# Kernel optimization log

Measured on AMD Instinct MI355X. Metric: run time of the kernel, lower is better.

Reference implementation:

```python
import jax, jax.numpy as jnp
import numpy as np

DIM = 50
K = 51  # kernel_size == DIM + 1 (required by the original view())
E = 6   # num_elems
NT = 29 # num_targets
B = 8
DN = ('NCDHW', 'OIDHW', 'NCDHW')


def setup_inputs() -> dict:
    key = jax.random.key(0)
    ks = jax.random.split(key, 14)
    f = jnp.float32
    inp = {
        'x': jax.random.uniform(ks[0], (B, E, DIM, DIM, DIM), dtype=f),
        'sigma': 3.0 * jnp.ones((E,), dtype=f),
        'w1': jax.random.normal(ks[1], (32, E, 3, 3, 3), dtype=f) * 0.1,
        'b1': jnp.full((32,), 0.01, dtype=f),
        'w2': jax.random.normal(ks[2], (64, 32, 3, 3, 3), dtype=f) * 0.05,
        'b2': jnp.full((64,), 0.01, dtype=f),
        'w3': jax.random.normal(ks[3], (128, 64, 3, 3, 3), dtype=f) * 0.05,
        'b3': jnp.full((128,), 0.01, dtype=f),
        'w4': jax.random.normal(ks[4], (256, 128, 3, 3, 3), dtype=f) * 0.03,
        'b4': jnp.full((256,), 0.01, dtype=f),
        'fw1': jax.random.normal(ks[5], (128, 256), dtype=f) * 0.06,
        'fb1': jnp.full((128,), 0.01, dtype=f),
        'fw2': jax.random.normal(ks[6], (NT, 128), dtype=f) * 0.08,
        'fb2': jnp.full((NT,), 0.01, dtype=f),
    }
    return inp


def _blur_kernel(sigma):
    # Gauss transformation kernel, shape (E, 1, K, K, K)
    c = jnp.arange(K, dtype=jnp.float32)
    mean = (K - 1) / 2.0
    d2 = (c - mean) ** 2
    # squared radius grid (K,K,K), symmetric so the torch transpose(3,0) axis swap is a no-op
    r2 = d2[:, None, None] + d2[None, :, None] + d2[None, None, :]
    var = sigma ** 2  # (E,)
    a = 1.0 / (2.0 * np.pi * var)  # (E,)
    kern = a[:, None, None, None] * jnp.exp(-r2[None] / (2.0 * var)[:, None, None, None])
    kern = kern / jnp.sum(kern)  # normalize by GLOBAL sum (as in torch code)
    return kern[:, None]  # (E,1,K,K,K)


def _conv3(x, w, b):
    y = jax.lax.conv_general_dilated(x, w, (1, 1, 1), 'VALID', dimension_numbers=DN)
    return y + b[None, :, None, None, None]


def _pool(x):
    return jax.lax.reduce_window(x, -jnp.inf, jax.lax.max,
                                 (1, 1, 2, 2, 2), (1, 1, 2, 2, 2), 'VALID')


def reference(x, sigma, w1, b1, w2, b2, w3, b3, w4, b4, fw1, fb1, fw2, fb2):
    # blur: grouped 3D conv with on-the-fly Gaussian kernel, padding 25 keeps DIM
    kern = _blur_kernel(sigma)
    pad = (K - 1) // 2
    xc = jax.lax.conv_general_dilated(x, kern, (1, 1, 1), [(pad, pad)] * 3,
                                      feature_group_count=E, dimension_numbers=DN)
    xc = xc / jnp.max(xc)
    # conv stack: (conv -> pool -> relu) x4
    h = jax.nn.relu(_pool(_conv3(xc, w1, b1)))   # (B,32,24,24,24)
    h = jax.nn.relu(_pool(_conv3(h, w2, b2)))    # (B,64,11,11,11)
    h = jax.nn.relu(_pool(_conv3(h, w3, b3)))    # (B,128,4,4,4)
    h = jax.nn.relu(_pool(_conv3(h, w4, b4)))    # (B,256,1,1,1)
    v = h.reshape(x.shape[0], -1)                # (B,256)
    y1 = jax.nn.relu(v @ fw1.T + fb1)
    return y1 @ fw2.T + fb2                      # (B,29)
```

## Files before the change

kernel.cpp:

```cpp
#include <hip/hip_runtime.h>
#include <math.h>

#define DIMX 50
#define KK   51
#define NE   6
#define NB   8
#define NVOX ((size_t)NB * NE * DIMX * DIMX * DIMX)

typedef short bf16x8 __attribute__((ext_vector_type(8)));
typedef float f32x4  __attribute__((ext_vector_type(4)));

__device__ __forceinline__ unsigned short f2bf(float f) {
    unsigned u = __float_as_uint(f);
    u += 0x7fffu + ((u >> 16) & 1u);
    return (unsigned short)(u >> 16);
}
__device__ __forceinline__ float bf2f(unsigned short h) {
    return __uint_as_float((unsigned)h << 16);
}
__device__ __forceinline__ uint4 pack8(const unsigned short v[8]) {
    uint4 q;
    q.x = v[0] | ((unsigned)v[1] << 16);
    q.y = v[2] | ((unsigned)v[3] << 16);
    q.z = v[4] | ((unsigned)v[5] << 16);
    q.w = v[6] | ((unsigned)v[7] << 16);
    return q;
}
__device__ __forceinline__ void split2(float v0, float v1, unsigned& hp, unsigned& lp) {
    unsigned u0 = __float_as_uint(v0), u1 = __float_as_uint(v1);
    float h0 = __uint_as_float(u0 & 0xffff0000u);
    float h1 = __uint_as_float(u1 & 0xffff0000u);
    hp = __builtin_amdgcn_perm(u1, u0, 0x07060302u);
    lp = __builtin_amdgcn_perm(__float_as_uint(v1 - h1), __float_as_uint(v0 - h0), 0x07060302u);
}
__device__ __forceinline__ int offA(int o, int k) {
    return ((((o >> 4) * 2 + (k >> 5)) * 64 + ((k >> 3) & 3) * 16 + (o & 15)) << 3) + (k & 7);
}

__global__ void taps_kernel(const float* __restrict__ sigma,
                            unsigned short* __restrict__ MA, unsigned short* __restrict__ MB,
                            float* __restrict__ maxval) {
    __shared__ float sg[NE * KK];
    __shared__ float sgs[NE * KK];
    __shared__ float ssum[NE];
    int t = threadIdx.x;
    if (t == 0) *maxval = 0.f;
    if (t < NE * KK) {
        int e = t / KK, i = t % KK;
        float d = (float)i - 25.0f;
        float var = sigma[e] * sigma[e];
        sg[t] = expf(-d * d / (2.f * var));
    }
    __syncthreads();
    if (t < NE) {
        float s = 0.f;
        for (int i = 0; i < KK; ++i) s += sg[t * KK + i];
        ssum[t] = s;
    }
    __syncthreads();
    if (t < NE * KK) {
        int e = t / KK;
        float S = 0.f;
        for (int e2 = 0; e2 < NE; ++e2) {
            float var2 = sigma[e2] * sigma[e2];
            float a2 = 1.f / (2.f * (float)M_PI * var2);
            float se = ssum[e2];
            S += a2 * se * se * se;
        }
        float var = sigma[e] * sigma[e];
        float a = 1.f / (2.f * (float)M_PI * var);
        sgs[t] = sg[t] * (a / S);
    }
    __syncthreads();
    const int TOT = 2 * 6 * 4 * 2 * 64 * 8;
    for (int i = t; i < 2 * TOT; i += 512) {
        int which = i / TOT;
        int r = i % TOT;
        int q = r;
        int j = q & 7; q >>= 3;
        int l = q & 63; q >>= 6;
        int kc = q & 1; q >>= 1;
        int tile = q & 3; q >>= 2;
        int e = q % 6; q /= 6;
        int hl = q;
        int own = tile * 16 + (l & 15);
        int k   = kc * 32 + ((l >> 4) << 3) + j;
        float v = 0.f;
        if (own < 50 && k < 50) {
            int d = k - own + 25;
            if (d >= 0 && d < KK) v = (which == 0 ? sg : sgs)[e * KK + d];
        }
        unsigned short h = f2bf(v);
        unsigned short out = (hl == 0) ? h : f2bf(v - bf2f(h));
        (which == 0 ? MA : MB)[r] = out;
    }
}

__global__ __launch_bounds__(64)
void blur_k1(const float* __restrict__ in, float* __restrict__ W1,
             const unsigned short* __restrict__ MA) {
    const int l = threadIdx.x, lm = l & 15, lg = l >> 4;
    const int y = blockIdx.x % 50, be = blockIdx.x / 50, e = be % 6;
    const float* pb = in + (size_t)be * 125000 + y * 50;
    bf16x8 Ah[4][2], Al[4][2];
#pragma unroll
    for (int ozt = 0; ozt < 4; ++ozt)
#pragma unroll
        for (int kc = 0; kc < 2; ++kc) {
            Ah[ozt][kc] = *(const bf16x8*)(MA + (((size_t)(0 * 6 + e) * 4 + ozt) * 2 + kc) * 512 + l * 8);
            Al[ozt][kc] = *(const bf16x8*)(MA + (((size_t)(1 * 6 + e) * 4 + ozt) * 2 + kc) * 512 + l * 8);
        }
    float* ob = W1 + (size_t)be * 125000 + y * 50;
    const f32x4 z4 = {0.f, 0.f, 0.f, 0.f};
#pragma unroll
    for (int xt = 0; xt < 4; ++xt) {
        const int xx = xt * 16 + lm;
        bf16x8 bh[2], bl[2];
#pragma unroll
        for (int kc = 0; kc < 2; ++kc) {
            float v[8];
#pragma unroll
            for (int j = 0; j < 8; ++j) {
                int z = kc * 32 + lg * 8 + j;
                v[j] = (z < 50 && xx < 50) ? pb[(size_t)z * 2500 + xx] : 0.f;
            }
            uint4 qh, ql;
            split2(v[0], v[1], qh.x, ql.x);
            split2(v[2], v[3], qh.y, ql.y);
            split2(v[4], v[5], qh.z, ql.z);
            split2(v[6], v[7], qh.w, ql.w);
            bh[kc] = *(bf16x8*)&qh; bl[kc] = *(bf16x8*)&ql;
        }
        f32x4 acc[4];
#pragma unroll
        for (int ozt = 0; ozt < 4; ++ozt) acc[ozt] = z4;
#pragma unroll
        for (int ozt = 0; ozt < 4; ++ozt)
#pragma unroll
            for (int kc = 0; kc < 2; ++kc) {
                acc[ozt] = __builtin_amdgcn_mfma_f32_16x16x32_bf16(Ah[ozt][kc], bh[kc], acc[ozt], 0, 0, 0);
                acc[ozt] = __builtin_amdgcn_mfma_f32_16x16x32_bf16(Ah[ozt][kc], bl[kc], acc[ozt], 0, 0, 0);
                acc[ozt] = __builtin_amdgcn_mfma_f32_16x16x32_bf16(Al[ozt][kc], bh[kc], acc[ozt], 0, 0, 0);
            }
        if (xx < 50) {
#pragma unroll
            for (int ozt = 0; ozt < 4; ++ozt)
#pragma unroll
                for (int i = 0; i < 4; ++i) {
                    int oz = ozt * 16 + lg * 4 + i;
                    if (oz < 50) ob[(size_t)oz * 2500 + xx] = acc[ozt][i];
                }
        }
    }
}

__global__ __launch_bounds__(64)
void blur_k2(const float* __restrict__ W1, const unsigned short* __restrict__ MA,
             const unsigned short* __restrict__ MB, unsigned short* __restrict__ X1,
             float* __restrict__ maxval) {
    __shared__ unsigned short Qhi[4096], Qlo[4096];
    const int l = threadIdx.x, lm = l & 15, lg = (l >> 4);
    const int q8 = (int)(gridDim.x >> 3);
    const int logical = ((int)blockIdx.x & 7) * q8 + ((int)blockIdx.x >> 3);
    const int e = logical % 6, bz = logical / 6, z = bz % 50, b = bz / 50;
    const float* pb = W1 + (size_t)(b * 6 + e) * 125000 + (size_t)z * 2500;
    bf16x8 Bh[4][2], Bl[4][2];
#pragma unroll
    for (int xt = 0; xt < 4; ++xt) {
        const int xx = xt * 16 + lm;
#pragma unroll
        for (int kc = 0; kc < 2; ++kc) {
            float v[8];
#pragma unroll
            for (int j = 0; j < 8; ++j) {
                int yy = kc * 32 + lg * 8 + j;
                v[j] = (yy < 50 && xx < 50) ? pb[yy * 50 + xx] : 0.f;
            }
            uint4 qh, ql;
            split2(v[0], v[1], qh.x, ql.x);
            split2(v[2], v[3], qh.y, ql.y);
            split2(v[4], v[5], qh.z, ql.z);
            split2(v[6], v[7], qh.w, ql.w);
            Bh[xt][kc] = *(bf16x8*)&qh; Bl[xt][kc] = *(bf16x8*)&ql;
        }
    }
    const f32x4 z4 = {0.f, 0.f, 0.f, 0.f};
#pragma unroll
    for (int oyt = 0; oyt < 4; ++oyt) {
        bf16x8 Ah[2], Al[2];
#pragma unroll
        for (int kc = 0; kc < 2; ++kc) {
            Ah[kc] = *(const bf16x8*)(MA + (((size_t)(0 * 6 + e) * 4 + oyt) * 2 + kc) * 512 + l * 8);
            Al[kc] = *(const bf16x8*)(MA + (((size_t)(1 * 6 + e) * 4 + oyt) * 2 + kc) * 512 + l * 8);
        }
#pragma unroll
        for (int xt = 0; xt < 4; ++xt) {
            f32x4 acc = z4;
#pragma unroll
            for (int kc = 0; kc < 2; ++kc) {
                acc = __builtin_amdgcn_mfma_f32_16x16x32_bf16(Ah[kc], Bh[xt][kc], acc, 0, 0, 0);
                acc = __builtin_amdgcn_mfma_f32_16x16x32_bf16(Ah[kc], Bl[xt][kc], acc, 0, 0, 0);
                acc = __builtin_amdgcn_mfma_f32_16x16x32_bf16(Al[kc], Bh[xt][kc], acc, 0, 0, 0);
            }
#pragma unroll
            for (int i = 0; i < 4; ++i) {
                int oy = oyt * 16 + lg * 4 + i;
                int xx = xt * 16 + lm;
                float qv = acc[i];
                unsigned u = __float_as_uint(qv);
                int off = offA(oy, xx);
                Qhi[off] = (unsigned short)(u >> 16);
                float lo = qv - __uint_as_float(u & 0xffff0000u);
                Qlo[off] = (unsigned short)(__float_as_uint(lo) >> 16);
            }
        }
    }
    __builtin_amdgcn_wave_barrier();
    asm volatile("s_waitcnt lgkmcnt(0)" ::: "memory");
    __builtin_amdgcn_sched_barrier(0);
    float mmax = 0.f;
    unsigned short* xb = X1 + ((size_t)b * 125000 + (size_t)z * 2500) * 8 + e;
#pragma unroll
    for (int oyt = 0; oyt < 4; ++oyt) {
        bf16x8 Qh[2], Ql[2];
#pragma unroll
        for (int kc = 0; kc < 2; ++kc) {
            Qh[kc] = *(const bf16x8*)(Qhi + ((oyt * 2 + kc) * 64 + l) * 8);
            Ql[kc] = *(const bf16x8*)(Qlo + ((oyt * 2 + kc) * 64 + l) * 8);
        }
#pragma unroll
        for (int oxt = 0; oxt < 4; ++oxt) {
            f32x4 acc = z4;
#pragma unroll
            for (int kc = 0; kc < 2; ++kc) {
                bf16x8 mh = *(const bf16x8*)(MB + (((size_t)(0 * 6 + e) * 4 + oxt) * 2 + kc) * 512 + l * 8);
                bf16x8 ml = *(const bf16x8*)(MB + (((size_t)(1 * 6 + e) * 4 + oxt) * 2 + kc) * 512 + l * 8);
                acc = __builtin_amdgcn_mfma_f32_16x16x32_bf16(Qh[kc], mh, acc, 0, 0, 0);
                acc = __builtin_amdgcn_mfma_f32_16x16x32_bf16(Qh[kc], ml, acc, 0, 0, 0);
                acc = __builtin_amdgcn_mfma_f32_16x16x32_bf16(Ql[kc], mh, acc, 0, 0, 0);
            }
            int ox = oxt * 16 + lm;
            if (ox < 50) {
#pragma unroll
                for (int i = 0; i < 4; ++i) {
                    int oy = oyt * 16 + lg * 4 + i;
                    if (oy < 50) {
                        float r = acc[i];
                        xb[((size_t)oy * 50 + ox) * 8] = f2bf(r);
                        mmax = fmaxf(mmax, r);
                    }
                }
            }
        }
    }
    for (int o = 32; o; o >>= 1) mmax = fmaxf(mmax, __shfl_xor(mmax, o));
    if (l == 0) atomicMax((int*)maxval, __float_as_int(mmax));
}

__global__ void wprep_all(const float* __restrict__ W1c, const float* __restrict__ W2c,
                          const float* __restrict__ W3c,
                          unsigned short* __restrict__ wp1, unsigned short* __restrict__ wp2,
                          unsigned short* __restrict__ wp3) {
    int idx = blockIdx.x * 256 + threadIdx.x;
    const int N1 = 2 * 9 * 64;
    const int N2 = 4 * 27 * 1 * 64;
    const int N3 = 8 * 27 * 2 * 64;
    if (idx < N1) {
        int l = idx & 63;
        int r = idx >> 6;
        int tg = r % 9, cog = r / 9;
        int xsel = l >> 4;
        int co = cog * 16 + (l & 15);
        unsigned short v[8];
#pragma unroll
        for (int j = 0; j < 8; ++j) {
            float wv = 0.f;
            if (j < 6 && xsel < 3) wv = W1c[((size_t)co * 6 + j) * 27 + tg * 3 + xsel];
            v[j] = f2bf(wv);
        }
        ((uint4*)wp1)[idx] = pack8(v);
        return;
    }
    idx -= N1;
    if (idx < N2) {
        int l = idx & 63;
        int r = idx >> 6;
        int tap = r % 27, cog = r / 27;
        int co = cog * 16 + (l & 15);
        unsigned short v[8];
#pragma unroll
        for (int j = 0; j < 8; ++j) {
            int ci = (l >> 4) * 8 + j;
            v[j] = f2bf(W2c[((size_t)co * 32 + ci) * 27 + tap]);
        }
        ((uint4*)wp2)[idx] = pack8(v);
        return;
    }
    idx -= N2;
    if (idx < N3) {
        int l = idx & 63;
        int r = idx >> 6;
        int ch = r % 2; r /= 2;
        int tap = r % 27;
        int cog = r / 27;
        int co = cog * 16 + (l & 15);
        unsigned short v[8];
#pragma unroll
        for (int j = 0; j < 8; ++j) {
            int ci = ch * 32 + (l >> 4) * 8 + j;
            v[j] = f2bf(W3c[((size_t)co * 64 + ci) * 27 + tap]);
        }
        ((uint4*)wp3)[idx] = pack8(v);
    }
}

__global__ __launch_bounds__(64, 3)
void conv1_mfma(const unsigned short* __restrict__ X8, const unsigned short* __restrict__ wp1,
                const float* __restrict__ bias, const float* __restrict__ maxval,
                unsigned short* __restrict__ X2) {
    const int l = threadIdx.x, lm = l & 15, lg = l >> 4;
    const int q = (int)(gridDim.x >> 3);
    const int bid = ((int)blockIdx.x & 7) * q + ((int)blockIdx.x >> 3);
    const int s0 = bid * 8;
    const int r0 = s0 / 72;
    const int cog = r0 % 2;
    const int pz  = (r0 / 2) % 24;
    const int b   = r0 / 48;
    uint4 B9[9];
    const uint4* wpb = (const uint4*)wp1 + cog * 9 * 64;
#pragma unroll
    for (int t = 0; t < 9; ++t) B9[t] = wpb[t * 64 + l];
    const float rmv = 1.0f / (*maxval);
    const float bia = bias[cog * 16 + lm];
    const unsigned short* Xb = X8 + (size_t)b * 125000 * 8;
    const f32x4 z4 = {0.f, 0.f, 0.f, 0.f};
#pragma unroll 1
    for (int si = 0; si < 8; ++si) {
        const int sid = s0 + si;
        const int xs = sid % 3;
        const int py = (sid / 3) % 24;
        const int x0 = xs * 16;
        f32x4 acc[2][2];
#pragma unroll
        for (int cz = 0; cz < 2; ++cz)
#pragma unroll
            for (int cy = 0; cy < 2; ++cy) acc[cz][cy] = z4;
#pragma unroll
        for (int zi = 0; zi < 4; ++zi) {
            const int zin = 2 * pz + zi;
#pragma unroll
            for (int yi = 0; yi < 4; ++yi) {
                const int yin = 2 * py + yi;
                const unsigned short* rowb = Xb + (size_t)(zin * 50 + yin) * 50 * 8;
                bf16x8 a = *(const bf16x8*)(rowb + (x0 + lm + lg) * 8);
#pragma unroll
                for (int cz = 0; cz < 2; ++cz) {
                    const int kz = zi - cz;
                    if (kz < 0 || kz > 2) continue;
#pragma unroll
                    for (int cy = 0; cy < 2; ++cy) {
                        const int ky = yi - cy;
                        if (ky < 0 || ky > 2) continue;
                        acc[cz][cy] = __builtin_amdgcn_mfma_f32_16x16x32_bf16(
                            a, *(const bf16x8*)&B9[kz * 3 + ky], acc[cz][cy], 0, 0, 0);
                    }
                }
            }
        }
        const int co = cog * 16 + lm;
#pragma unroll
        for (int ip = 0; ip < 2; ++ip) {
            float m0 = fmaxf(fmaxf(acc[0][0][2 * ip], acc[0][1][2 * ip]),
                             fmaxf(acc[1][0][2 * ip], acc[1][1][2 * ip]));
            float m1 = fmaxf(fmaxf(acc[0][0][2 * ip + 1], acc[0][1][2 * ip + 1]),
                             fmaxf(acc[1][0][2 * ip + 1], acc[1][1][2 * ip + 1]));
            float o = fmaxf(fmaxf(m0, m1) * rmv + bia, 0.f);
            int px = x0 / 2 + lg * 2 + ip;
            X2[((((size_t)b * 24 + pz) * 24 + py) * 24 + px) * 32 + co] = f2bf(o);
        }
    }
}

template <int DIN, int DP, int CI, int NCH, int NCOG, int NPY, int NXS, int SPB, int NPZ>
__global__ __launch_bounds__(64, 3)
void convN_mfma(const unsigned short* __restrict__ X, const unsigned short* __restrict__ wp,
                const float* __restrict__ bias, unsigned short* __restrict__ Y, int COUT) {
    const int l = threadIdx.x, lm = l & 15, lg = l >> 4;
    const int qq = (int)(gridDim.x >> 3);
    const int bid = ((int)blockIdx.x & 7) * qq + ((int)blockIdx.x >> 3);
    const int s0 = bid * SPB;
    const int r0 = s0 / (NPY * NXS);
    const int cog = r0 % NCOG;
    const int pz  = (r0 / NCOG) % NPZ;
    const int b   = r0 / (NCOG * NPZ);
    const float bia = bias[cog * 16 + lm];
    const unsigned short* Xb = X + (size_t)b * DIN * DIN * DIN * CI;
    const uint4* wp4 = (const uint4*)wp;
    const f32x4 z4 = {0.f, 0.f, 0.f, 0.f};
#pragma unroll 1
    for (int si = 0; si < SPB; ++si) {
        const int sid = s0 + si;
        const int xs = sid % NXS;
        const int py = (sid / NXS) % NPY;
        const int x0 = xs * 16;
        int xo[3];
#pragma unroll
        for (int kx = 0; kx < 3; ++kx) {
            int xin = x0 + kx + lm;
            if (xin > DIN - 1) xin = DIN - 1;
            xo[kx] = xin * CI + lg * 8;
        }
        f32x4 acc[2][2];
#pragma unroll
        for (int cz = 0; cz < 2; ++cz)
#pragma unroll
            for (int cy = 0; cy < 2; ++cy) acc[cz][cy] = z4;
#pragma unroll 1
        for (int ch = 0; ch < NCH; ++ch) {
            uint4 B[27];
            const uint4* wpb = wp4 + ((size_t)cog * 27 * NCH + ch) * 64;
#pragma unroll
            for (int t = 0; t < 27; ++t) B[t] = wpb[(size_t)t * NCH * 64 + l];
            const unsigned short* Xc = Xb + ch * 32;
#pragma unroll
            for (int zi = 0; zi < 4; ++zi) {
                const int zin = 2 * pz + zi;
#pragma unroll
                for (int yi = 0; yi < 4; ++yi) {
                    const int yin = 2 * py + yi;
                    const unsigned short* rowb = Xc + (size_t)(zin * DIN + yin) * DIN * CI;
#pragma unroll
                    for (int kx = 0; kx < 3; ++kx) {
                        bf16x8 a = *(const bf16x8*)(rowb + xo[kx]);
#pragma unroll
                        for (int cz = 0; cz < 2; ++cz) {
                            const int kz = zi - cz;
                            if (kz < 0 || kz > 2) continue;
#pragma unroll
                            for (int cy = 0; cy < 2; ++cy) {
                                const int ky = yi - cy;
                                if (ky < 0 || ky > 2) continue;
                                const int tap = (kz * 3 + ky) * 3 + kx;
                                acc[cz][cy] = __builtin_amdgcn_mfma_f32_16x16x32_bf16(
                                    a, *(const bf16x8*)&B[tap], acc[cz][cy], 0, 0, 0);
                            }
                        }
                    }
                }
            }
        }
        const int co = cog * 16 + lm;
#pragma unroll
        for (int ip = 0; ip < 2; ++ip) {
            float m0 = fmaxf(fmaxf(acc[0][0][2 * ip], acc[0][1][2 * ip]),
                             fmaxf(acc[1][0][2 * ip], acc[1][1][2 * ip]));
            float m1 = fmaxf(fmaxf(acc[0][0][2 * ip + 1], acc[0][1][2 * ip + 1]),
                             fmaxf(acc[1][0][2 * ip + 1], acc[1][1][2 * ip + 1]));
            float o = fmaxf(fmaxf(m0, m1) + bia, 0.f);
            int px = x0 / 2 + lg * 2 + ip;
            if (px < DP)
                Y[((((size_t)b * DP + pz) * DP + py) * DP + px) * COUT + co] = f2bf(o);
        }
    }
}

__global__ void conv4_kernel(const unsigned short* __restrict__ X4, const float* __restrict__ w,
                             const float* __restrict__ bias, float* __restrict__ out) {
    int wid = (int)((blockIdx.x * blockDim.x + threadIdx.x) >> 6);
    int lane = threadIdx.x & 63;
    if (wid >= NB * 256) return;
    int b = wid >> 8, co = wid & 255;
    float acc[8];
#pragma unroll
    for (int i = 0; i < 8; ++i) acc[i] = 0.f;
    for (int half = 0; half < 2; ++half) {
        int ci = lane + half * 64;
        float win[64];
#pragma unroll
        for (int v = 0; v < 64; ++v)
            win[v] = bf2f(X4[((size_t)b * 64 + v) * 128 + ci]);
        const float* wc = w + ((size_t)co * 128 + ci) * 27;
        float wr[27];
#pragma unroll
        for (int i = 0; i < 27; ++i) wr[i] = wc[i];
#pragma unroll
        for (int kz = 0; kz < 3; ++kz)
#pragma unroll
            for (int ky = 0; ky < 3; ++ky)
#pragma unroll
                for (int kx = 0; kx < 3; ++kx) {
                    float wv = wr[(kz * 3 + ky) * 3 + kx];
#pragma unroll
                    for (int oz = 0; oz < 2; ++oz)
#pragma unroll
                        for (int oy = 0; oy < 2; ++oy)
#pragma unroll
                            for (int ox = 0; ox < 2; ++ox)
                                acc[(oz * 2 + oy) * 2 + ox] =
                                    fmaf(wv, win[((oz + kz) * 4 + (oy + ky)) * 4 + ox + kx],
                                         acc[(oz * 2 + oy) * 2 + ox]);
                }
    }
#pragma unroll
    for (int o = 32; o; o >>= 1)
#pragma unroll
        for (int i = 0; i < 8; ++i) acc[i] += __shfl_xor(acc[i], o);
    if (lane == 0) {
        float m = acc[0];
#pragma unroll
        for (int i = 1; i < 8; ++i) m = fmaxf(m, acc[i]);
        out[(size_t)b * 256 + co] = fmaxf(m + bias[co], 0.f);
    }
}

__global__ void head_kernel(const float* __restrict__ v,
                            const float* __restrict__ fw1, const float* __restrict__ fb1,
                            const float* __restrict__ fw2, const float* __restrict__ fb2,
                            float* __restrict__ out) {
    int b = blockIdx.x, t = threadIdx.x;
    __shared__ float sv[256];
    __shared__ float s1[128];
    sv[t] = v[b * 256 + t];
    sv[t + 128] = v[b * 256 + t + 128];
    __syncthreads();
    float acc = fb1[t];
    const float* wr = fw1 + t * 256;
    for (int k = 0; k < 256; ++k) acc = fmaf(wr[k], sv[k], acc);
    s1[t] = fmaxf(acc, 0.f);
    __syncthreads();
    if (t < 29) {
        float a2 = fb2[t];
        const float* w2 = fw2 + t * 128;
        for (int k = 0; k < 128; ++k) a2 = fmaf(w2[k], s1[k], a2);
        out[b * 29 + t] = a2;
    }
}

extern "C" void kernel_launch(void* const* d_in, const int* in_sizes, int n_in,
                              void* d_out, int out_size, void* d_ws, size_t ws_size,
                              hipStream_t stream) {
    const float* x     = (const float*)d_in[0];
    const float* sigma = (const float*)d_in[1];
    const float* w1    = (const float*)d_in[2];
    const float* b1    = (const float*)d_in[3];
    const float* w2    = (const float*)d_in[4];
    const float* b2    = (const float*)d_in[5];
    const float* w3    = (const float*)d_in[6];
    const float* b3    = (const float*)d_in[7];
    const float* w4    = (const float*)d_in[8];
    const float* b4    = (const float*)d_in[9];
    const float* fw1   = (const float*)d_in[10];
    const float* fb1   = (const float*)d_in[11];
    const float* fw2   = (const float*)d_in[12];
    const float* fb2   = (const float*)d_in[13];
    float* out = (float*)d_out;

    float* W1 = (float*)d_ws;
    unsigned short* X1  = (unsigned short*)(W1 + NVOX);
    unsigned short* X2  = X1 + 8000064;
    unsigned short* X3  = X2 + 3538944;
    unsigned short* X4  = X3 + 681472;
    unsigned short* wp1 = X4 + 65536;
    unsigned short* wp2 = wp1 + 9216;
    unsigned short* wp3 = wp2 + 55296;
    unsigned short* MA  = wp3 + 221184;
    unsigned short* MB  = MA + 49152;
    float* mx = (float*)(MB + 49152);
    float* v4 = mx + 1;

    taps_kernel<<<1, 512, 0, stream>>>(sigma, MA, MB, mx);

    blur_k1<<<NB * NE * 50, 64, 0, stream>>>(x, W1, MA);
    blur_k2<<<NB * NE * 50, 64, 0, stream>>>(W1, MA, MB, X1, mx);

    wprep_all<<<140, 256, 0, stream>>>(w1, w2, w3, wp1, wp2, wp3);

    conv1_mfma<<<3456, 64, 0, stream>>>(X1, wp1, b1, mx, X2);
    convN_mfma<24, 11, 32, 1, 4, 11, 2, 2, 11><<<3872, 64, 0, stream>>>(X2, wp2, b2, X3, 64);
    convN_mfma<11, 4, 64, 2, 8, 4, 1, 1, 4><<<1024, 64, 0, stream>>>(X3, wp3, b3, X4, 128);

    conv4_kernel<<<512, 256, 0, stream>>>(X4, w4, b4, v4);
    head_kernel<<<8, 128, 0, stream>>>(v4, fw1, fb1, fw2, fb2, out);
}
```

Before: 196.3 us.

## Split blur kernels four ways across output tiles for more blocks

Both separable-blur kernels now launch four times as many single-wave blocks, each handling one 16-wide tile (x tile in blur_k1, oy tile in blur_k2) instead of looping over all four. This raises the number of waves available to hide memory latency and shrinks LDS use per block in blur_k2. In exchange, blur_k2 reloads the full 50x50 input plane and recomputes its first-stage B fragments in every one of the four blocks, and the max atomic is issued four times as often.

Result: slower. 269.4 us (+37.2%).

```diff
diff --git a/kernel.cpp b/kernel.cpp
--- a/kernel.cpp
+++ b/kernel.cpp
@@ -33,8 +33,8 @@
     hp = __builtin_amdgcn_perm(u1, u0, 0x07060302u);
     lp = __builtin_amdgcn_perm(__float_as_uint(v1 - h1), __float_as_uint(v0 - h0), 0x07060302u);
 }
-__device__ __forceinline__ int offA(int o, int k) {
-    return ((((o >> 4) * 2 + (k >> 5)) * 64 + ((k >> 3) & 3) * 16 + (o & 15)) << 3) + (k & 7);
+__device__ __forceinline__ int offA2(int o, int k) {
+    return ((((k >> 5) * 64) + ((k >> 3) & 3) * 16 + (o & 15)) << 3) + (k & 7);
 }
 
 __global__ void taps_kernel(const float* __restrict__ sigma,
@@ -100,56 +100,46 @@
 void blur_k1(const float* __restrict__ in, float* __restrict__ W1,
              const unsigned short* __restrict__ MA) {
     const int l = threadIdx.x, lm = l & 15, lg = l >> 4;
-    const int y = blockIdx.x % 50, be = blockIdx.x / 50, e = be % 6;
+    const int xt = (int)blockIdx.x & 3;
+    const int r = (int)blockIdx.x >> 2;
+    const int y = r % 50, be = r / 50, e = be % 6;
     const float* pb = in + (size_t)be * 125000 + y * 50;
-    bf16x8 Ah[4][2], Al[4][2];
-#pragma unroll
-    for (int ozt = 0; ozt < 4; ++ozt)
-#pragma unroll
-        for (int kc = 0; kc < 2; ++kc) {
-            Ah[ozt][kc] = *(const bf16x8*)(MA + (((size_t)(0 * 6 + e) * 4 + ozt) * 2 + kc) * 512 + l * 8);
-            Al[ozt][kc] = *(const bf16x8*)(MA + (((size_t)(1 * 6 + e) * 4 + ozt) * 2 + kc) * 512 + l * 8);
-        }
     float* ob = W1 + (size_t)be * 125000 + y * 50;
     const f32x4 z4 = {0.f, 0.f, 0.f, 0.f};
-#pragma unroll
-    for (int xt = 0; xt < 4; ++xt) {
-        const int xx = xt * 16 + lm;
-        bf16x8 bh[2], bl[2];
+    const int xx = xt * 16 + lm;
+    bf16x8 bh[2], bl[2];
+#pragma unroll
+    for (int kc = 0; kc < 2; ++kc) {
+        float v[8];
+#pragma unroll
+        for (int j = 0; j < 8; ++j) {
+            int z = kc * 32 + lg * 8 + j;
+            v[j] = (z < 50 && xx < 50) ? pb[(size_t)z * 2500 + xx] : 0.f;
+        }
+        uint4 qh, ql;
+        split2(v[0], v[1], qh.x, ql.x);
+        split2(v[2], v[3], qh.y, ql.y);
+        split2(v[4], v[5], qh.z, ql.z);
+        split2(v[6], v[7], qh.w, ql.w);
+        bh[kc] = *(bf16x8*)&qh; bl[kc] = *(bf16x8*)&ql;
+    }
+#pragma unroll
+    for (int ozt = 0; ozt < 4; ++ozt) {
+        f32x4 acc = z4;
 #pragma unroll
         for (int kc = 0; kc < 2; ++kc) {
-            float v[8];
-#pragma unroll
-            for (int j = 0; j < 8; ++j) {
-                int z = kc * 32 + lg * 8 + j;
-                v[j] = (z < 50 && xx < 50) ? pb[(size_t)z * 2500 + xx] : 0.f;
-            }
-            uint4 qh, ql;
-            split2(v[0], v[1], qh.x, ql.x);
-            split2(v[2], v[3], qh.y, ql.y);
-            split2(v[4], v[5], qh.z, ql.z);
-            split2(v[6], v[7], qh.w, ql.w);
-            bh[kc] = *(bf16x8*)&qh; bl[kc] = *(bf16x8*)&ql;
-        }
-        f32x4 acc[4];
-#pragma unroll
-        for (int ozt = 0; ozt < 4; ++ozt) acc[ozt] = z4;
-#pragma unroll
-        for (int ozt = 0; ozt < 4; ++ozt)
-#pragma unroll
-            for (int kc = 0; kc < 2; ++kc) {
-                acc[ozt] = __builtin_amdgcn_mfma_f32_16x16x32_bf16(Ah[ozt][kc], bh[kc], acc[ozt], 0, 0, 0);
-                acc[ozt] = __builtin_amdgcn_mfma_f32_16x16x32_bf16(Ah[ozt][kc], bl[kc], acc[ozt], 0, 0, 0);
-                acc[ozt] = __builtin_amdgcn_mfma_f32_16x16x32_bf16(Al[ozt][kc], bh[kc], acc[ozt], 0, 0, 0);
-            }
+            bf16x8 Ah = *(const bf16x8*)(MA + (((size_t)(0 * 6 + e) * 4 + ozt) * 2 + kc) * 512 + l * 8);
+            bf16x8 Al = *(const bf16x8*)(MA + (((size_t)(1 * 6 + e) * 4 + ozt) * 2 + kc) * 512 + l * 8);
+            acc = __builtin_amdgcn_mfma_f32_16x16x32_bf16(Ah, bh[kc], acc, 0, 0, 0);
+            acc = __builtin_amdgcn_mfma_f32_16x16x32_bf16(Ah, bl[kc], acc, 0, 0, 0);
+            acc = __builtin_amdgcn_mfma_f32_16x16x32_bf16(Al, bh[kc], acc, 0, 0, 0);
+        }
         if (xx < 50) {
 #pragma unroll
-            for (int ozt = 0; ozt < 4; ++ozt)
-#pragma unroll
-                for (int i = 0; i < 4; ++i) {
-                    int oz = ozt * 16 + lg * 4 + i;
-                    if (oz < 50) ob[(size_t)oz * 2500 + xx] = acc[ozt][i];
-                }
+            for (int i = 0; i < 4; ++i) {
+                int oz = ozt * 16 + lg * 4 + i;
+                if (oz < 50) ob[(size_t)oz * 2500 + xx] = acc[i];
+            }
         }
     }
 }
@@ -158,11 +148,13 @@
 void blur_k2(const float* __restrict__ W1, const unsigned short* __restrict__ MA,
              const unsigned short* __restrict__ MB, unsigned short* __restrict__ X1,
              float* __restrict__ maxval) {
-    __shared__ unsigned short Qhi[4096], Qlo[4096];
+    __shared__ unsigned short Qhi[1024], Qlo[1024];
     const int l = threadIdx.x, lm = l & 15, lg = (l >> 4);
     const int q8 = (int)(gridDim.x >> 3);
     const int logical = ((int)blockIdx.x & 7) * q8 + ((int)blockIdx.x >> 3);
-    const int e = logical % 6, bz = logical / 6, z = bz % 50, b = bz / 50;
+    const int oyt = logical & 3;
+    const int r = logical >> 2;
+    const int e = r % 6, bz = r / 6, z = bz % 50, b = bz / 50;
     const float* pb = W1 + (size_t)(b * 6 + e) * 125000 + (size_t)z * 2500;
     bf16x8 Bh[4][2], Bl[4][2];
 #pragma unroll
@@ -185,8 +177,7 @@
         }
     }
     const f32x4 z4 = {0.f, 0.f, 0.f, 0.f};
-#pragma unroll
-    for (int oyt = 0; oyt < 4; ++oyt) {
+    {
         bf16x8 Ah[2], Al[2];
 #pragma unroll
         for (int kc = 0; kc < 2; ++kc) {
@@ -208,7 +199,7 @@
                 int xx = xt * 16 + lm;
                 float qv = acc[i];
                 unsigned u = __float_as_uint(qv);
-                int off = offA(oy, xx);
+                int off = offA2(oy, xx);
                 Qhi[off] = (unsigned short)(u >> 16);
                 float lo = qv - __uint_as_float(u & 0xffff0000u);
                 Qlo[off] = (unsigned short)(__float_as_uint(lo) >> 16);
@@ -220,35 +211,32 @@
     __builtin_amdgcn_sched_barrier(0);
     float mmax = 0.f;
     unsigned short* xb = X1 + ((size_t)b * 125000 + (size_t)z * 2500) * 8 + e;
-#pragma unroll
-    for (int oyt = 0; oyt < 4; ++oyt) {
-        bf16x8 Qh[2], Ql[2];
+    bf16x8 Qh[2], Ql[2];
+#pragma unroll
+    for (int kc = 0; kc < 2; ++kc) {
+        Qh[kc] = *(const bf16x8*)(Qhi + (kc * 64 + l) * 8);
+        Ql[kc] = *(const bf16x8*)(Qlo + (kc * 64 + l) * 8);
+    }
+#pragma unroll
+    for (int oxt = 0; oxt < 4; ++oxt) {
+        f32x4 acc = z4;
 #pragma unroll
         for (int kc = 0; kc < 2; ++kc) {
-            Qh[kc] = *(const bf16x8*)(Qhi + ((oyt * 2 + kc) * 64 + l) * 8);
-            Ql[kc] = *(const bf16x8*)(Qlo + ((oyt * 2 + kc) * 64 + l) * 8);
-        }
-#pragma unroll
-        for (int oxt = 0; oxt < 4; ++oxt) {
-            f32x4 acc = z4;
-#pragma unroll
-            for (int kc = 0; kc < 2; ++kc) {
-                bf16x8 mh = *(const bf16x8*)(MB + (((size_t)(0 * 6 + e) * 4 + oxt) * 2 + kc) * 512 + l * 8);
-                bf16x8 ml = *(const bf16x8*)(MB + (((size_t)(1 * 6 + e) * 4 + oxt) * 2 + kc) * 512 + l * 8);
-                acc = __builtin_amdgcn_mfma_f32_16x16x32_bf16(Qh[kc], mh, acc, 0, 0, 0);
-                acc = __builtin_amdgcn_mfma_f32_16x16x32_bf16(Qh[kc], ml, acc, 0, 0, 0);
-                acc = __builtin_amdgcn_mfma_f32_16x16x32_bf16(Ql[kc], mh, acc, 0, 0, 0);
-            }
-            int ox = oxt * 16 + lm;
-            if (ox < 50) {
-#pragma unroll
-                for (int i = 0; i < 4; ++i) {
-                    int oy = oyt * 16 + lg * 4 + i;
-                    if (oy < 50) {
-                        float r = acc[i];
-                        xb[((size_t)oy * 50 + ox) * 8] = f2bf(r);
-                        mmax = fmaxf(mmax, r);
-                    }
+            bf16x8 mh = *(const bf16x8*)(MB + (((size_t)(0 * 6 + e) * 4 + oxt) * 2 + kc) * 512 + l * 8);
+            bf16x8 ml = *(const bf16x8*)(MB + (((size_t)(1 * 6 + e) * 4 + oxt) * 2 + kc) * 512 + l * 8);
+            acc = __builtin_amdgcn_mfma_f32_16x16x32_bf16(Qh[kc], mh, acc, 0, 0, 0);
+            acc = __builtin_amdgcn_mfma_f32_16x16x32_bf16(Qh[kc], ml, acc, 0, 0, 0);
+            acc = __builtin_amdgcn_mfma_f32_16x16x32_bf16(Ql[kc], mh, acc, 0, 0, 0);
+        }
+        int ox = oxt * 16 + lm;
+        if (ox < 50) {
+#pragma unroll
+            for (int i = 0; i < 4; ++i) {
+                int oy = oyt * 16 + lg * 4 + i;
+                if (oy < 50) {
+                    float rv = acc[i];
+                    xb[((size_t)oy * 50 + ox) * 8] = f2bf(rv);
+                    mmax = fmaxf(mmax, rv);
                 }
             }
         }
@@ -570,8 +558,8 @@
 
     taps_kernel<<<1, 512, 0, stream>>>(sigma, MA, MB, mx);
 
-    blur_k1<<<NB * NE * 50, 64, 0, stream>>>(x, W1, MA);
-    blur_k2<<<NB * NE * 50, 64, 0, stream>>>(W1, MA, MB, X1, mx);
+    blur_k1<<<NB * NE * 50 * 4, 64, 0, stream>>>(x, W1, MA);
+    blur_k2<<<NB * NE * 50 * 4, 64, 0, stream>>>(W1, MA, MB, X1, mx);
 
     wprep_all<<<140, 256, 0, stream>>>(w1, w2, w3, wp1, wp2, wp3);
 
```
